# Optimization experiments

Hardware: AMD Instinct MI355X
Metric: run time of the kernel (lower is better)

The kernel has to match this reference:

```python
import jax, jax.numpy as jnp
import numpy as np

N_NODES = 10000
N_EDGES = 320000


def setup_inputs() -> dict:
    key = jax.random.key(0)
    ks = jax.random.split(key, 8)
    node_features = jax.random.normal(ks[0], (N_NODES, 128), dtype=jnp.float32)
    edge_src = jax.random.randint(ks[1], (N_EDGES,), 0, N_NODES, dtype=jnp.int32)
    edge_dst = jax.random.randint(ks[2], (N_EDGES,), 0, N_NODES, dtype=jnp.int32)
    # QCNN params: Linear(128->256)+Tanh, Linear(256->256)+Tanh, then sigmoid; out Linear(256->128)
    W1 = jax.random.normal(ks[3], (128, 256), dtype=jnp.float32) / np.sqrt(128)
    b1 = jnp.zeros((256,), dtype=jnp.float32)
    W2 = jax.random.normal(ks[4], (256, 256), dtype=jnp.float32) / np.sqrt(256)
    b2 = jnp.zeros((256,), dtype=jnp.float32)
    Wo = jax.random.normal(ks[5], (256, 128), dtype=jnp.float32) / np.sqrt(256)
    bo = jnp.zeros((128,), dtype=jnp.float32)
    return dict(node_features=node_features, edge_src=edge_src, edge_dst=edge_dst,
                W1=W1, b1=b1, W2=W2, b2=b2, Wo=Wo, bo=bo)


def reference(node_features, edge_src, edge_dst, W1, b1, W2, b2, Wo, bo):
    # QCNN dense encoder: tanh MLP followed by sigmoid
    h = jnp.tanh(node_features @ W1 + b1)        # [N, 256]
    h = jnp.tanh(h @ W2 + b2)                    # [N, 256]
    hidden = jax.nn.sigmoid(h)                   # [N, 256]
    # Neighbor mean aggregation (segment mean over incoming edges).
    # Nodes with no neighbors keep zeros, matching the torch loop.
    sums = jax.ops.segment_sum(hidden[edge_src], edge_dst, num_segments=N_NODES)  # [N, 256]
    deg = jax.ops.segment_sum(jnp.ones_like(edge_dst, dtype=hidden.dtype), edge_dst,
                              num_segments=N_NODES)                              # [N]
    agg = sums / jnp.maximum(deg, 1.0)[:, None]
    return agg @ Wo + bo                         # [N, 128]
```

## Files before the change

### kernel.cpp

```cpp
#include <hip/hip_runtime.h>
#include <hip/hip_bf16.h>

#define NN 10000
#define NE 320000

typedef __attribute__((ext_vector_type(8))) short bf16x8;
typedef __attribute__((ext_vector_type(4))) float f32x4;
typedef __attribute__((ext_vector_type(8))) unsigned short ushort8;

__device__ inline void split_bf16(float a, unsigned short& hi, unsigned short& lo) {
  union { float f; unsigned int u; } v; v.f = a;
  hi = (unsigned short)(v.u >> 16);
  union { float f; unsigned int u; } h; h.u = (unsigned int)hi << 16;
  float r = a - h.f;
  union { float f; unsigned int u; } w; w.f = r;
  lo = (unsigned short)(w.u >> 16);
}

__global__ __launch_bounds__(256) void convertx_kernel(
    const float* __restrict__ X, unsigned short* __restrict__ Xhi,
    unsigned short* __restrict__ Xlo) {
  int i = blockIdx.x * 256 + threadIdx.x;
  float a = X[i];
  unsigned short h, l; split_bf16(a, h, l);
  Xhi[i] = h; Xlo[i] = l;
}

template<int K, int N>
__global__ __launch_bounds__(256) void prepw_kernel(
    const float* __restrict__ W, unsigned short* __restrict__ Thi,
    unsigned short* __restrict__ Tlo) {
  int e = blockIdx.x * 256 + threadIdx.x;
  if (e >= K * N) return;
  int k = e / N, n = e % N;
  unsigned short h, l; split_bf16(W[e], h, l);
  Thi[n * K + k] = h; Tlo[n * K + k] = l;
}

template<int ACT, bool BIAS_, int OUTM, int K, int N>
__global__ __launch_bounds__(256) void mfma_gemm(
    const unsigned short* __restrict__ Ahi_g, const unsigned short* __restrict__ Alo_g,
    const unsigned short* __restrict__ Bthi_g, const unsigned short* __restrict__ Btlo_g,
    const float* __restrict__ bias, float* __restrict__ Cf,
    unsigned short* __restrict__ Chi, unsigned short* __restrict__ Clo, int M) {
  __shared__ unsigned short Ah[64 * 64], Al[64 * 64], Bh[64 * 64], Bl[64 * 64];

  const int tid = threadIdx.x;
  const int lane = tid & 63;
  const int wid = tid >> 6;
  const int wr = wid >> 1, wc = wid & 1;
  const int row0 = blockIdx.x * 64;
  const int col0 = blockIdx.y * 64;

  f32x4 acc[2][2];
#pragma unroll
  for (int m = 0; m < 2; m++)
#pragma unroll
    for (int n = 0; n < 2; n++) acc[m][n] = (f32x4){0.f, 0.f, 0.f, 0.f};

  for (int kt = 0; kt < K / 64; ++kt) {
#pragma unroll
    for (int it = 0; it < 2; ++it) {
      int c = it * 256 + tid;
      int r = c >> 3, cj = c & 7;
      int dj = (cj ^ (r & 7)) * 8;
      int grow = row0 + r; if (grow > M - 1) grow = M - 1;
      size_t ga = (size_t)grow * K + kt * 64 + cj * 8;
      *(ushort8*)&Ah[r * 64 + dj] = *(const ushort8*)&Ahi_g[ga];
      *(ushort8*)&Al[r * 64 + dj] = *(const ushort8*)&Alo_g[ga];
      size_t gb = (size_t)(col0 + r) * K + kt * 64 + cj * 8;
      *(ushort8*)&Bh[r * 64 + dj] = *(const ushort8*)&Bthi_g[gb];
      *(ushort8*)&Bl[r * 64 + dj] = *(const ushort8*)&Btlo_g[gb];
    }
    __syncthreads();
#pragma unroll
    for (int kk = 0; kk < 2; ++kk) {
      bf16x8 aH[2], aL[2], bH[2], bL[2];
#pragma unroll
      for (int m = 0; m < 2; m++) {
        int row = wr * 32 + m * 16 + (lane & 15);
        int ch = (kk * 4 + (lane >> 4)) ^ (row & 7);
        aH[m] = *(const bf16x8*)&Ah[row * 64 + ch * 8];
        aL[m] = *(const bf16x8*)&Al[row * 64 + ch * 8];
      }
#pragma unroll
      for (int n = 0; n < 2; n++) {
        int col = wc * 32 + n * 16 + (lane & 15);
        int ch = (kk * 4 + (lane >> 4)) ^ (col & 7);
        bH[n] = *(const bf16x8*)&Bh[col * 64 + ch * 8];
        bL[n] = *(const bf16x8*)&Bl[col * 64 + ch * 8];
      }
#pragma unroll
      for (int m = 0; m < 2; m++)
#pragma unroll
        for (int n = 0; n < 2; n++) {
          acc[m][n] = __builtin_amdgcn_mfma_f32_16x16x32_bf16(aH[m], bH[n], acc[m][n], 0, 0, 0);
          acc[m][n] = __builtin_amdgcn_mfma_f32_16x16x32_bf16(aH[m], bL[n], acc[m][n], 0, 0, 0);
          acc[m][n] = __builtin_amdgcn_mfma_f32_16x16x32_bf16(aL[m], bH[n], acc[m][n], 0, 0, 0);
        }
    }
    __syncthreads();
  }

#pragma unroll
  for (int m = 0; m < 2; m++)
#pragma unroll
    for (int n = 0; n < 2; n++) {
      int col = col0 + wc * 32 + n * 16 + (lane & 15);
      float bv = BIAS_ ? bias[col] : 0.f;
#pragma unroll
      for (int j = 0; j < 4; j++) {
        int row = row0 + wr * 32 + m * 16 + (lane >> 4) * 4 + j;
        if (row < M) {
          float v = acc[m][n][j] + bv;
          if (ACT == 1) v = tanhf(v);
          else if (ACT == 2) v = 1.f / (1.f + expf(-tanhf(v)));
          if (OUTM == 0) {
            Cf[(size_t)row * N + col] = v;
          } else {
            unsigned short h, l; split_bf16(v, h, l);
            Chi[(size_t)row * N + col] = h;
            Clo[(size_t)row * N + col] = l;
          }
        }
      }
    }
}

__global__ void count_kernel(const int* __restrict__ dst, int* __restrict__ deg, int n) {
  int i = blockIdx.x * blockDim.x + threadIdx.x;
  if (i < n) atomicAdd(&deg[dst[i]], 1);
}

__global__ __launch_bounds__(1024) void scan_kernel(
    const int* __restrict__ deg, int* __restrict__ offs, int* __restrict__ cursor) {
  __shared__ int wsum[16];
  int t = threadIdx.x;
  int base = t * 10;
  int loc[10];
  int s = 0;
  if (base < NN) {
#pragma unroll
    for (int i = 0; i < 10; i++) {
      int idx = base + i;
      int v = (idx < NN) ? deg[idx] : 0;
      loc[i] = s; s += v;
    }
  }
  int lane = t & 63, w = t >> 6;
  int incl = s;
  for (int off = 1; off < 64; off <<= 1) {
    int u = __shfl_up(incl, off, 64);
    if (lane >= off) incl += u;
  }
  if (lane == 63) wsum[w] = incl;
  __syncthreads();
  if (t == 0) {
    int c = 0;
#pragma unroll
    for (int i = 0; i < 16; i++) { int v = wsum[i]; wsum[i] = c; c += v; }
  }
  __syncthreads();
  int ex = wsum[w] + incl - s;
  if (base < NN) {
#pragma unroll
    for (int i = 0; i < 10; i++) {
      int idx = base + i;
      if (idx < NN) { int o = ex + loc[i]; offs[idx] = o; cursor[idx] = o; }
    }
  }
}

__global__ void fill_kernel(const int* __restrict__ src, const int* __restrict__ dst,
                            int* __restrict__ cursor, int* __restrict__ csr, int n) {
  int i = blockIdx.x * blockDim.x + threadIdx.x;
  if (i < n) {
    int d = dst[i];
    int pos = atomicAdd(&cursor[d], 1);
    csr[pos] = src[i];
  }
}

__global__ __launch_bounds__(256) void aggregate_kernel(
    const float* __restrict__ hproj, const int* __restrict__ csr,
    const int* __restrict__ offs, const int* __restrict__ deg,
    const float* __restrict__ bo, float* __restrict__ out, int n_nodes) {
  int wave = threadIdx.x >> 6;
  int lane = threadIdx.x & 63;
  int node = blockIdx.x * 4 + wave;
  if (node >= n_nodes) return;
  int start = offs[node];
  int d = deg[node];
  const float2* h2 = (const float2*)hproj;
  float2 acc = make_float2(0.f, 0.f);
  int t = 0;
  for (; t + 4 <= d; t += 4) {
    int s0 = csr[start + t + 0];
    int s1 = csr[start + t + 1];
    int s2 = csr[start + t + 2];
    int s3 = csr[start + t + 3];
    float2 v0 = h2[s0 * 64 + lane];
    float2 v1 = h2[s1 * 64 + lane];
    float2 v2 = h2[s2 * 64 + lane];
    float2 v3 = h2[s3 * 64 + lane];
    acc.x += (v0.x + v1.x) + (v2.x + v3.x);
    acc.y += (v0.y + v1.y) + (v2.y + v3.y);
  }
  for (; t < d; t++) {
    int s = csr[start + t];
    float2 v = h2[s * 64 + lane];
    acc.x += v.x; acc.y += v.y;
  }
  float scale = 1.f / fmaxf((float)d, 1.f);
  float2 b = ((const float2*)bo)[lane];
  float2 o = make_float2(fmaf(acc.x, scale, b.x), fmaf(acc.y, scale, b.y));
  ((float2*)out)[node * 64 + lane] = o;
}

extern "C" void kernel_launch(void* const* d_in, const int* in_sizes, int n_in,
                              void* d_out, int out_size, void* d_ws, size_t ws_size,
                              hipStream_t stream) {
  const float* X    = (const float*)d_in[0];
  const int*   esrc = (const int*)d_in[1];
  const int*   edst = (const int*)d_in[2];
  const float* W1   = (const float*)d_in[3];
  const float* b1   = (const float*)d_in[4];
  const float* W2   = (const float*)d_in[5];
  const float* b2   = (const float*)d_in[6];
  const float* Wo   = (const float*)d_in[7];
  const float* bo   = (const float*)d_in[8];
  float* out = (float*)d_out;

  char* p = (char*)d_ws;
  size_t needed = (size_t)NN * 256 * 4 * 2
                + (size_t)(32768 + 65536 + 32768) * 2 * 2
                + (size_t)(3 * NN + NE) * 4;
  if (ws_size < needed) return;

  unsigned short* regA  = (unsigned short*)p;
  unsigned short* Xhi   = regA;
  unsigned short* Xlo   = regA + (size_t)NN * 128;
  unsigned short* hidhi = regA;
  unsigned short* hidlo = regA + (size_t)NN * 256;
  p += (size_t)NN * 256 * 4;
  unsigned short* h1hi  = (unsigned short*)p;
  unsigned short* h1lo  = h1hi + (size_t)NN * 256;
  float*          hproj = (float*)h1hi;
  p += (size_t)NN * 256 * 4;
  unsigned short* W1thi = (unsigned short*)p; p += 32768 * 2;
  unsigned short* W1tlo = (unsigned short*)p; p += 32768 * 2;
  unsigned short* W2thi = (unsigned short*)p; p += 65536 * 2;
  unsigned short* W2tlo = (unsigned short*)p; p += 65536 * 2;
  unsigned short* Wothi = (unsigned short*)p; p += 32768 * 2;
  unsigned short* Wotlo = (unsigned short*)p; p += 32768 * 2;
  int* deg    = (int*)p; p += (size_t)NN * 4;
  int* offs   = (int*)p; p += (size_t)NN * 4;
  int* cursor = (int*)p; p += (size_t)NN * 4;
  int* csr    = (int*)p; p += (size_t)NE * 4;

  hipMemsetAsync(deg, 0, NN * sizeof(int), stream);

  count_kernel<<<(NE + 255) / 256, 256, 0, stream>>>(edst, deg, NE);
  scan_kernel<<<1, 1024, 0, stream>>>(deg, offs, cursor);
  fill_kernel<<<(NE + 255) / 256, 256, 0, stream>>>(esrc, edst, cursor, csr, NE);

  convertx_kernel<<<NN * 128 / 256, 256, 0, stream>>>(X, Xhi, Xlo);
  prepw_kernel<128, 256><<<(128 * 256 + 255) / 256, 256, 0, stream>>>(W1, W1thi, W1tlo);
  prepw_kernel<256, 256><<<(256 * 256 + 255) / 256, 256, 0, stream>>>(W2, W2thi, W2tlo);
  prepw_kernel<256, 128><<<(256 * 128 + 255) / 256, 256, 0, stream>>>(Wo, Wothi, Wotlo);

  mfma_gemm<1, true, 1, 128, 256><<<dim3(157, 4), 256, 0, stream>>>(
      Xhi, Xlo, W1thi, W1tlo, b1, nullptr, h1hi, h1lo, NN);
  mfma_gemm<2, true, 1, 256, 256><<<dim3(157, 4), 256, 0, stream>>>(
      h1hi, h1lo, W2thi, W2tlo, b2, nullptr, hidhi, hidlo, NN);
  mfma_gemm<0, false, 0, 256, 128><<<dim3(157, 2), 256, 0, stream>>>(
      hidhi, hidlo, Wothi, Wotlo, nullptr, hproj, nullptr, nullptr, NN);

  aggregate_kernel<<<(NN + 3) / 4, 256, 0, stream>>>(hproj, csr, offs, deg, bo, out, NN);
}
```

Baseline: 185.2 us.

## Fuse prep kernels and memset, batch CSR index loads with shuffles in aggregation

Merges the deg memset, X conversion and three weight-transpose kernels into a single prep kernel, replacing five launches with one and vectorising the X split to float4. The weight transpose now reads strided and writes coalesced. The aggregation kernel loads up to 64 CSR indices per wave in one coalesced read, broadcasts them with shuffles, and unrolls the gather by 8 with two accumulators for more loads in flight. The cost is extra shuffle instructions and a slightly changed float summation order.

```diff
diff --git a/kernel.cpp b/kernel.cpp
--- a/kernel.cpp
+++ b/kernel.cpp
@@ -17,24 +17,47 @@
   lo = (unsigned short)(w.u >> 16);
 }
 
-__global__ __launch_bounds__(256) void convertx_kernel(
+__global__ __launch_bounds__(256) void prep_kernel(
     const float* __restrict__ X, unsigned short* __restrict__ Xhi,
-    unsigned short* __restrict__ Xlo) {
+    unsigned short* __restrict__ Xlo,
+    const float* __restrict__ W1, unsigned short* __restrict__ W1thi,
+    unsigned short* __restrict__ W1tlo,
+    const float* __restrict__ W2, unsigned short* __restrict__ W2thi,
+    unsigned short* __restrict__ W2tlo,
+    const float* __restrict__ Wo, unsigned short* __restrict__ Wothi,
+    unsigned short* __restrict__ Wotlo,
+    int* __restrict__ deg) {
   int i = blockIdx.x * 256 + threadIdx.x;
-  float a = X[i];
-  unsigned short h, l; split_bf16(a, h, l);
-  Xhi[i] = h; Xlo[i] = l;
-}
-
-template<int K, int N>
-__global__ __launch_bounds__(256) void prepw_kernel(
-    const float* __restrict__ W, unsigned short* __restrict__ Thi,
-    unsigned short* __restrict__ Tlo) {
-  int e = blockIdx.x * 256 + threadIdx.x;
-  if (e >= K * N) return;
-  int k = e / N, n = e % N;
-  unsigned short h, l; split_bf16(W[e], h, l);
-  Thi[n * K + k] = h; Tlo[n * K + k] = l;
+
+  if (i < 2500) ((int4*)deg)[i] = make_int4(0, 0, 0, 0);
+
+  {
+    float4 x = ((const float4*)X)[i];
+    ushort4 h, l;
+    split_bf16(x.x, h.x, l.x);
+    split_bf16(x.y, h.y, l.y);
+    split_bf16(x.z, h.z, l.z);
+    split_bf16(x.w, h.w, l.w);
+    ((ushort4*)Xhi)[i] = h;
+    ((ushort4*)Xlo)[i] = l;
+  }
+
+  if (i < 32768) {
+    int n = i >> 7, k = i & 127;
+    unsigned short h, l; split_bf16(W1[k * 256 + n], h, l);
+    W1thi[i] = h; W1tlo[i] = l;
+  }
+  if (i < 65536) {
+    int n = i >> 8, k = i & 255;
+    unsigned short h, l; split_bf16(W2[k * 256 + n], h, l);
+    W2thi[i] = h; W2tlo[i] = l;
+  }
+  if (i >= 65536 && i < 98304) {
+    int o = i - 65536;
+    int n = o >> 8, k = o & 255;
+    unsigned short h, l; split_bf16(Wo[k * 128 + n], h, l);
+    Wothi[o] = h; Wotlo[o] = l;
+  }
 }
 
 template<int ACT, bool BIAS_, int OUTM, int K, int N>
@@ -192,28 +215,36 @@
   int start = offs[node];
   int d = deg[node];
   const float2* h2 = (const float2*)hproj;
-  float2 acc = make_float2(0.f, 0.f);
-  int t = 0;
-  for (; t + 4 <= d; t += 4) {
-    int s0 = csr[start + t + 0];
-    int s1 = csr[start + t + 1];
-    int s2 = csr[start + t + 2];
-    int s3 = csr[start + t + 3];
-    float2 v0 = h2[s0 * 64 + lane];
-    float2 v1 = h2[s1 * 64 + lane];
-    float2 v2 = h2[s2 * 64 + lane];
-    float2 v3 = h2[s3 * 64 + lane];
-    acc.x += (v0.x + v1.x) + (v2.x + v3.x);
-    acc.y += (v0.y + v1.y) + (v2.y + v3.y);
-  }
-  for (; t < d; t++) {
-    int s = csr[start + t];
-    float2 v = h2[s * 64 + lane];
-    acc.x += v.x; acc.y += v.y;
+  float2 acc0 = make_float2(0.f, 0.f), acc1 = make_float2(0.f, 0.f);
+  for (int t0 = 0; t0 < d; t0 += 64) {
+    int rem = d - t0; if (rem > 64) rem = 64;
+    int idx = (lane < rem) ? csr[start + t0 + lane] : 0;
+    int j = 0;
+    for (; j + 8 <= rem; j += 8) {
+      int s0 = __shfl(idx, j + 0), s1 = __shfl(idx, j + 1);
+      int s2 = __shfl(idx, j + 2), s3 = __shfl(idx, j + 3);
+      int s4 = __shfl(idx, j + 4), s5 = __shfl(idx, j + 5);
+      int s6 = __shfl(idx, j + 6), s7 = __shfl(idx, j + 7);
+      float2 v0 = h2[s0 * 64 + lane], v1 = h2[s1 * 64 + lane];
+      float2 v2 = h2[s2 * 64 + lane], v3 = h2[s3 * 64 + lane];
+      float2 v4 = h2[s4 * 64 + lane], v5 = h2[s5 * 64 + lane];
+      float2 v6 = h2[s6 * 64 + lane], v7 = h2[s7 * 64 + lane];
+      acc0.x += (v0.x + v1.x) + (v2.x + v3.x);
+      acc0.y += (v0.y + v1.y) + (v2.y + v3.y);
+      acc1.x += (v4.x + v5.x) + (v6.x + v7.x);
+      acc1.y += (v4.y + v5.y) + (v6.y + v7.y);
+    }
+    for (; j < rem; j++) {
+      int s = __shfl(idx, j);
+      float2 v = h2[s * 64 + lane];
+      acc0.x += v.x; acc0.y += v.y;
+    }
   }
   float scale = 1.f / fmaxf((float)d, 1.f);
   float2 b = ((const float2*)bo)[lane];
-  float2 o = make_float2(fmaf(acc.x, scale, b.x), fmaf(acc.y, scale, b.y));
+  float2 o;
+  o.x = fmaf(acc0.x + acc1.x, scale, b.x);
+  o.y = fmaf(acc0.y + acc1.y, scale, b.y);
   ((float2*)out)[node * 64 + lane] = o;
 }
 
@@ -258,16 +289,12 @@
   int* cursor = (int*)p; p += (size_t)NN * 4;
   int* csr    = (int*)p; p += (size_t)NE * 4;
 
-  hipMemsetAsync(deg, 0, NN * sizeof(int), stream);
+  prep_kernel<<<1250, 256, 0, stream>>>(X, Xhi, Xlo, W1, W1thi, W1tlo,
+                                        W2, W2thi, W2tlo, Wo, Wothi, Wotlo, deg);
 
   count_kernel<<<(NE + 255) / 256, 256, 0, stream>>>(edst, deg, NE);
   scan_kernel<<<1, 1024, 0, stream>>>(deg, offs, cursor);
   fill_kernel<<<(NE + 255) / 256, 256, 0, stream>>>(esrc, edst, cursor, csr, NE);
-
-  convertx_kernel<<<NN * 128 / 256, 256, 0, stream>>>(X, Xhi, Xlo);
-  prepw_kernel<128, 256><<<(128 * 256 + 255) / 256, 256, 0, stream>>>(W1, W1thi, W1tlo);
-  prepw_kernel<256, 256><<<(256 * 256 + 255) / 256, 256, 0, stream>>>(W2, W2thi, W2tlo);
-  prepw_kernel<256, 128><<<(256 * 128 + 255) / 256, 256, 0, stream>>>(Wo, Wothi, Wotlo);
 
   mfma_gemm<1, true, 1, 128, 256><<<dim3(157, 4), 256, 0, stream>>>(
       Xhi, Xlo, W1thi, W1tlo, b1, nullptr, h1hi, h1lo, NN);
```

Result: faster. 174.6 us (-5.7%).
